# Performance work log

Measured on AMD Instinct MI355X. Metric: run time of the kernel, lower is better.

Reference implementation:

```python
import jax, jax.numpy as jnp
import numpy as np

_SAMPLING_EPS = 1e-05
_RMAX = 0.9999999403953552          # largest float32 uniform from tl.rand
_RMAX_LOG = -5.960464477539063e-08  # log(_RMAX)


def setup_inputs() -> dict:
    key = jax.random.key(0)
    k1, k2, k3, k4, k5 = jax.random.split(key, 5)
    B, V = 256, 128000
    logits = jax.random.normal(k1, (B, V), dtype=jnp.float32) * 4.0
    temperature = jax.random.uniform(k2, (B,), dtype=jnp.float32, minval=0.1, maxval=1.5)
    top_k = jax.random.randint(k3, (B,), 1, 1000).astype(jnp.int32)
    top_p = jax.random.uniform(k4, (B,), dtype=jnp.float32, minval=0.5, maxval=1.0)
    gumbel_u = jax.random.uniform(k5, (B, V), dtype=jnp.float32)
    return {
        "logits": logits,
        "temperature": temperature,
        "top_k": top_k,
        "top_p": top_p,
        "gumbel_u": gumbel_u,
        "num_logprobs": 20,
    }


def reference(logits, temperature, top_k, top_p, gumbel_u, num_logprobs):
    B, V = logits.shape
    # --- apply_temperature: divide by temp, temp<eps treated as 1.0 (greedy) ---
    temp = jnp.where(temperature < _SAMPLING_EPS, 1.0, temperature)
    logits = logits.astype(jnp.float32) / temp[:, None]

    # --- apply_top_k_top_p: sort ascending, mask, scatter back ---
    idx_sort = jnp.argsort(logits, axis=-1)                      # ascending
    logits_sort = jnp.take_along_axis(logits, idx_sort, axis=-1)
    # top-k: value of the k-th largest is at position V-k in ascending order
    k_pos = (V - top_k.astype(jnp.int32))[:, None]
    thresh = jnp.take_along_axis(logits_sort, k_pos, axis=-1)    # [B,1]
    logits_sort = jnp.where(logits_sort < thresh, -jnp.inf, logits_sort)
    # top-p: drop ascending prefix whose cumulative prob <= 1-p (keep last)
    probs_sort = jax.nn.softmax(logits_sort, axis=-1)
    cum = jnp.cumsum(probs_sort, axis=-1)
    mask_p = cum <= (1.0 - top_p)[:, None]
    mask_p = mask_p.at[:, -1].set(False)
    logits_sort = jnp.where(mask_p, -jnp.inf, logits_sort)
    # unsort back to vocab order
    inv = jnp.argsort(idx_sort, axis=-1)
    logits_f = jnp.take_along_axis(logits_sort, inv, axis=-1)

    # --- softmax + gumbel-trick sampling: argmax(p / -log(u)) ---
    probs = jax.nn.softmax(logits_f, axis=-1)
    q = -jnp.where(gumbel_u >= _RMAX, _RMAX_LOG, jnp.log(gumbel_u))
    greedy = (temperature < _SAMPLING_EPS)[:, None]  # kernel skips these rows
    ratio = jnp.where(greedy, probs, probs / q)
    sampled = jnp.argmax(ratio, axis=-1)             # [B]

    # --- gather_logprobs ---
    logprobs = jax.nn.log_softmax(logits_f, axis=-1)
    sampled_lp = jnp.take_along_axis(logprobs, sampled[:, None], axis=-1)  # [B,1]
    ranks = jnp.sum(logprobs > sampled_lp, axis=-1)                        # [B]
    topk_lp, topk_idx = jax.lax.top_k(logprobs, num_logprobs)
    indices = jnp.concatenate([sampled[:, None], topk_idx], axis=1)        # [B,1+K]
    lp_vals = jnp.concatenate([sampled_lp, topk_lp], axis=1)               # [B,1+K]

    return sampled[:, None], indices, lp_vals, ranks
```

## Files before the change

kernel.cpp:

```cpp
#include <hip/hip_runtime.h>
#include <math.h>

#define NTHR 1024
#define CAP 8192
#define BINS 4096
#define SMALL 1024
#define GUARD 16u
#define SS 4096

#define RMAX_F 0.9999999403953552f
#define RMAX_LOG_F -5.960464477539063e-08f
#define NEG_BIG -3.0e38f

__device__ __forceinline__ unsigned keyOf(float v) {
    unsigned b = __float_as_uint(v);
    return (b & 0x80000000u) ? ~b : (b | 0x80000000u);
}
__device__ __forceinline__ float valOfKey(unsigned k) {
    unsigned b = (k & 0x80000000u) ? (k ^ 0x80000000u) : ~k;
    return __uint_as_float(b);
}
__device__ __forceinline__ unsigned long long shflXor64(unsigned long long v, int m) {
    int lo = __shfl_xor((int)(unsigned)v, m);
    int hi = __shfl_xor((int)(unsigned)(v >> 32), m);
    return ((unsigned long long)(unsigned)hi << 32) | (unsigned)lo;
}

__global__ __launch_bounds__(NTHR) void sampler_kernel(
    const float* __restrict__ logits,
    const float* __restrict__ temperature,
    const int* __restrict__ top_kv,
    const float* __restrict__ top_pv,
    const float* __restrict__ gumbel,
    float* __restrict__ out,
    int B, int V, int K)
{
    const int r = blockIdx.x;
    const int tid = threadIdx.x;
    const int lane = tid & 63;
    const int wid = tid >> 6;

    __shared__ unsigned long long cand[CAP];
    __shared__ unsigned long long cand2[SMALL];
    __shared__ unsigned refHist[512];
    __shared__ int wtotI[16];
    __shared__ float varr[1024];
    __shared__ float Earr[1024];
    __shared__ float sfx[1024];
    __shared__ unsigned char flagArr[1024];
    __shared__ unsigned bitmap[64];
    __shared__ unsigned s_prefix;
    __shared__ int s_cntgt, s_total, s_lvl;
    __shared__ int s_ncand, s_nc2, s_nkeep, s_rank, s_g0, s_g1;
    __shared__ unsigned long long s_amax;
    __shared__ float s_vs;

    unsigned* hist = (unsigned*)cand;

    const float* row = logits + (long long)r * V;
    const float* urow = gumbel + (long long)r * V;

    float traw = temperature[r];
    bool greedy = traw < 1e-5f;
    float t = greedy ? 1.0f : traw;
    int k = top_kv[r];
    if (k < 1) k = 1;
    if (k > V) k = V;
    float p = top_pv[r];

    const float4* row4 = (const float4*)row;
    const int V4 = V >> 2;
    const int Vt = V4 << 2;
    const unsigned cpy = tid & 1u;

#define H4(v4) do { \
        atomicAdd(&hist[((keyOf((v4).x) >> 20) << 1) | cpy], 1u); \
        atomicAdd(&hist[((keyOf((v4).y) >> 20) << 1) | cpy], 1u); \
        atomicAdd(&hist[((keyOf((v4).z) >> 20) << 1) | cpy], 1u); \
        atomicAdd(&hist[((keyOf((v4).w) >> 20) << 1) | cpy], 1u); \
    } while (0)
#define SPEC1(val, gidx_, thr_) do { \
        float _v = (val); \
        if (_v >= (thr_)) { \
            int _pos = atomicAdd(&s_ncand, 1); \
            if (_pos < CAP) \
                cand[_pos] = ((unsigned long long)keyOf(_v) << 32) | (unsigned)(~(unsigned)(gidx_)); \
        } \
    } while (0)

    for (int i = tid; i < BINS * 2; i += NTHR) hist[i] = 0;
    __syncthreads();
    {
        int f4pos = (int)(((long long)tid * V4) >> 10);
        float4 sv = row4[f4pos];
        H4(sv);
    }
    __syncthreads();
    int ts;
    {
        int tc = 3 * k + 500;
        if (tc > 3500) tc = 3500;
        if (tc < 700) tc = 700;
        ts = (int)(((long long)tc * SS + V - 1) / V);
        if (ts < 4) ts = 4;
    }
    {
        int base = tid << 2;
        int cs = 0;
        #pragma unroll
        for (int j = 0; j < 4; ++j)
            cs += (int)(hist[(base + j) * 2] + hist[(base + j) * 2 + 1]);
        int vv = cs;
        #pragma unroll
        for (int d = 1; d < 64; d <<= 1) {
            int o = __shfl_down(vv, d);
            if (lane + d < 64) vv += o;
        }
        if (lane == 0) wtotI[wid] = vv;
        __syncthreads();
        int off = 0;
        for (int w = wid + 1; w < 16; ++w) off += wtotI[w];
        int mine = vv + off;
        int above = mine - cs;
        if (mine >= ts && above < ts) {
            int run = above;
            for (int b = base + 3; b >= base; --b) {
                int mb = (int)(hist[b * 2] + hist[b * 2 + 1]);
                if (run + mb >= ts) { s_prefix = (unsigned)b; break; }
                run += mb;
            }
        }
        if (tid == 0) s_ncand = 0;
        __syncthreads();
    }
    unsigned tlo = s_prefix << 20;
    float thrF = valOfKey(tlo);

    {
        int i = tid;
        for (; i + 3 * NTHR < V4; i += 4 * NTHR) {
            float4 a = row4[i];
            float4 b = row4[i + NTHR];
            float4 c = row4[i + 2 * NTHR];
            float4 d = row4[i + 3 * NTHR];
            SPEC1(a.x, i * 4 + 0, thrF); SPEC1(a.y, i * 4 + 1, thrF);
            SPEC1(a.z, i * 4 + 2, thrF); SPEC1(a.w, i * 4 + 3, thrF);
            SPEC1(b.x, (i + NTHR) * 4 + 0, thrF); SPEC1(b.y, (i + NTHR) * 4 + 1, thrF);
            SPEC1(b.z, (i + NTHR) * 4 + 2, thrF); SPEC1(b.w, (i + NTHR) * 4 + 3, thrF);
            SPEC1(c.x, (i + 2 * NTHR) * 4 + 0, thrF); SPEC1(c.y, (i + 2 * NTHR) * 4 + 1, thrF);
            SPEC1(c.z, (i + 2 * NTHR) * 4 + 2, thrF); SPEC1(c.w, (i + 2 * NTHR) * 4 + 3, thrF);
            SPEC1(d.x, (i + 3 * NTHR) * 4 + 0, thrF); SPEC1(d.y, (i + 3 * NTHR) * 4 + 1, thrF);
            SPEC1(d.z, (i + 3 * NTHR) * 4 + 2, thrF); SPEC1(d.w, (i + 3 * NTHR) * 4 + 3, thrF);
        }
        for (; i < V4; i += NTHR) {
            float4 a = row4[i];
            SPEC1(a.x, i * 4 + 0, thrF); SPEC1(a.y, i * 4 + 1, thrF);
            SPEC1(a.z, i * 4 + 2, thrF); SPEC1(a.w, i * 4 + 3, thrF);
        }
        for (int ii = Vt + tid; ii < V; ii += NTHR)
            SPEC1(row[ii], ii, thrF);
    }
    __syncthreads();
    int ncand = s_ncand;
    const bool fastok = (ncand >= k && ncand <= CAP);

    if (!fastok) {
        for (int i = tid; i < BINS * 2; i += NTHR) hist[i] = 0;
        __syncthreads();
        {
            int i = tid;
            for (; i + 3 * NTHR < V4; i += 4 * NTHR) {
                float4 a = row4[i];
                float4 b = row4[i + NTHR];
                float4 c = row4[i + 2 * NTHR];
                float4 d = row4[i + 3 * NTHR];
                H4(a); H4(b); H4(c); H4(d);
            }
            for (; i < V4; i += NTHR) { float4 a = row4[i]; H4(a); }
            for (int ii = Vt + tid; ii < V; ii += NTHR)
                atomicAdd(&hist[((keyOf(row[ii]) >> 20) << 1) | cpy], 1u);
        }
        __syncthreads();
        {
            int base = tid << 2;
            int cs = 0;
            #pragma unroll
            for (int j = 0; j < 4; ++j)
                cs += (int)(hist[(base + j) * 2] + hist[(base + j) * 2 + 1]);
            int vv = cs;
            #pragma unroll
            for (int d = 1; d < 64; d <<= 1) {
                int o = __shfl_down(vv, d);
                if (lane + d < 64) vv += o;
            }
            if (lane == 0) wtotI[wid] = vv;
            __syncthreads();
            int off = 0;
            for (int w = wid + 1; w < 16; ++w) off += wtotI[w];
            int mine = vv + off;
            int above = mine - cs;
            if (mine >= k && above < k) {
                int run = above;
                for (int b = base + 3; b >= base; --b) {
                    int mb = (int)(hist[b * 2] + hist[b * 2 + 1]);
                    if (run + mb >= k) {
                        s_prefix = (unsigned)b; s_cntgt = run; s_total = run + mb; s_lvl = 0;
                        break;
                    }
                    run += mb;
                }
            }
        }
        for (int level = 1; level <= 2; ++level) {
            __syncthreads();
            if (s_total <= CAP) break;
            for (int i = tid; i < 512; i += NTHR) hist[i] = 0;
            __syncthreads();
            unsigned pfx = s_prefix;
            const int msh = 32 - (12 + 8 * (level - 1));
            const int bsh = msh - 8;
            for (int i = tid; i < V4; i += NTHR) {
                float4 l4 = row4[i];
                float vv4[4] = { l4.x, l4.y, l4.z, l4.w };
                #pragma unroll
                for (int j = 0; j < 4; ++j) {
                    unsigned key = keyOf(vv4[j]);
                    if ((key >> msh) == pfx)
                        atomicAdd(&hist[(((key >> bsh) & 255u) << 1) | cpy], 1u);
                }
            }
            for (int i = Vt + tid; i < V; i += NTHR) {
                unsigned key = keyOf(row[i]);
                if ((key >> msh) == pfx)
                    atomicAdd(&hist[(((key >> bsh) & 255u) << 1) | cpy], 1u);
            }
            __syncthreads();
            if (tid == 0) {
                int run = s_cntgt;
                for (int b = 255; b >= 0; --b) {
                    int mb = (int)(hist[b * 2] + hist[b * 2 + 1]);
                    if (run + mb >= k) {
                        s_prefix = (pfx << 8) | (unsigned)b; s_cntgt = run; s_total = run + mb;
                        break;
                    }
                    run += mb;
                }
                s_lvl = level;
            }
        }
        __syncthreads();
        tlo = s_prefix << (20 - 8 * s_lvl);
        thrF = valOfKey(tlo);
        if (tid == 0) s_ncand = 0;
        __syncthreads();
        {
            int i = tid;
            for (; i + 3 * NTHR < V4; i += 4 * NTHR) {
                float4 a = row4[i];
                float4 b = row4[i + NTHR];
                float4 c = row4[i + 2 * NTHR];
                float4 d = row4[i + 3 * NTHR];
                SPEC1(a.x, i * 4 + 0, thrF); SPEC1(a.y, i * 4 + 1, thrF);
                SPEC1(a.z, i * 4 + 2, thrF); SPEC1(a.w, i * 4 + 3, thrF);
                SPEC1(b.x, (i + NTHR) * 4 + 0, thrF); SPEC1(b.y, (i + NTHR) * 4 + 1, thrF);
                SPEC1(b.z, (i + NTHR) * 4 + 2, thrF); SPEC1(b.w, (i + NTHR) * 4 + 3, thrF);
                SPEC1(c.x, (i + 2 * NTHR) * 4 + 0, thrF); SPEC1(c.y, (i + 2 * NTHR) * 4 + 1, thrF);
                SPEC1(c.z, (i + 2 * NTHR) * 4 + 2, thrF); SPEC1(c.w, (i + 2 * NTHR) * 4 + 3, thrF);
                SPEC1(d.x, (i + 3 * NTHR) * 4 + 0, thrF); SPEC1(d.y, (i + 3 * NTHR) * 4 + 1, thrF);
                SPEC1(d.z, (i + 3 * NTHR) * 4 + 2, thrF); SPEC1(d.w, (i + 3 * NTHR) * 4 + 3, thrF);
            }
            for (; i < V4; i += NTHR) {
                float4 a = row4[i];
                SPEC1(a.x, i * 4 + 0, thrF); SPEC1(a.y, i * 4 + 1, thrF);
                SPEC1(a.z, i * 4 + 2, thrF); SPEC1(a.w, i * 4 + 3, thrF);
            }
            for (int ii = Vt + tid; ii < V; ii += NTHR)
                SPEC1(row[ii], ii, thrF);
        }
        __syncthreads();
        ncand = s_ncand;
        if (ncand > CAP) ncand = CAP;
        if (k > ncand) k = ncand;
    }
    if (k > ncand) k = ncand;

    bool fromC2 = false;
    bool bigSort = false;
    if (ncand > SMALL) {
        unsigned pfx; int run; int bb;
        if (fastok) { pfx = 0u; run = 0; bb = 32; }
        else { pfx = s_prefix; run = s_cntgt; bb = 20 - 8 * s_lvl; }
        while (bb > 0) {
            int step = (bb >= 8) ? 8 : bb;
            bb -= step;
            int nbins = 1 << step;
            for (int i = tid; i < nbins * 2; i += NTHR) refHist[i] = 0;
            __syncthreads();
            {
                int sh = bb + step;
                for (int i = tid; i < ncand; i += NTHR) {
                    unsigned key = (unsigned)(cand[i] >> 32);
                    bool in = (sh >= 32) || ((key >> sh) == pfx);
                    if (in)
                        atomicAdd(&refHist[(((key >> bb) & (unsigned)(nbins - 1)) << 1) | cpy], 1u);
                }
            }
            __syncthreads();
            int cnt = 0;
            if (tid < 256) cnt = (tid < nbins) ? (int)(refHist[tid * 2] + refHist[tid * 2 + 1]) : 0;
            int vv = cnt;
            #pragma unroll
            for (int d = 1; d < 64; d <<= 1) {
                int o = __shfl_down(vv, d);
                if (lane + d < 64) vv += o;
            }
            if (tid < 256 && lane == 0) wtotI[wid] = vv;
            __syncthreads();
            if (tid < 256) {
                int off = 0;
                for (int w = wid + 1; w < 4; ++w) off += wtotI[w];
                int incl = vv + off;
                int abv = incl - cnt;
                int kk = k - run;
                if (incl >= kk && abv < kk) {
                    s_prefix = (pfx << step) | (unsigned)tid;
                    s_cntgt = run + abv;
                }
            }
            __syncthreads();
            pfx = s_prefix;
            run = s_cntgt;
        }
        unsigned tref = (pfx >= tlo + GUARD) ? (pfx - GUARD) : tlo;
        if (tid == 0) s_nc2 = 0;
        __syncthreads();
        for (int i = tid; i < ncand; i += NTHR) {
            unsigned long long cv = cand[i];
            bool pred = ((unsigned)(cv >> 32) >= tref);
            unsigned long long mask = __ballot(pred ? 1 : 0);
            if (mask) {
                int leader = __ffsll(mask) - 1;
                int cnt2 = __popcll(mask);
                int bpos = 0;
                if (lane == leader) bpos = atomicAdd(&s_nc2, cnt2);
                bpos = __shfl(bpos, leader);
                if (pred) {
                    int pos = bpos + __popcll(mask & ((1ULL << lane) - 1ULL));
                    if (pos < SMALL) cand2[pos] = cv;
                }
            }
        }
        __syncthreads();
        int nc2 = s_nc2;
        if (nc2 <= SMALL) { ncand = nc2; fromC2 = true; }
        else bigSort = true;
    }

    if (!bigSort) {
        const unsigned long long* src = fromC2 ? cand2 : cand;
        unsigned long long v = (tid < ncand) ? src[tid] : 0ULL;
        #pragma unroll
        for (int size = 2; size <= SMALL; size <<= 1) {
            #pragma unroll
            for (int stride = size >> 1; stride > 0; stride >>= 1) {
                unsigned long long o;
                if (stride < 64) {
                    o = shflXor64(v, stride);
                } else {
                    cand[tid] = v;
                    __syncthreads();
                    o = cand[tid ^ stride];
                    __syncthreads();
                }
                bool takeMax = (((tid & size) == 0) == ((tid & stride) == 0));
                unsigned long long mx = (v > o) ? v : o;
                unsigned long long mn = (v > o) ? o : v;
                v = takeMax ? mx : mn;
            }
        }
        cand[tid] = v;
        varr[tid] = (tid < ncand) ? (valOfKey((unsigned)(v >> 32)) / t) : NEG_BIG;
        __syncthreads();
    } else {
        int P = 2; while (P < ncand) P <<= 1;
        for (int i = ncand + tid; i < P; i += NTHR) cand[i] = 0ULL;
        __syncthreads();
        for (int size = 2; size <= P; size <<= 1) {
            for (int stride = size >> 1; stride > 0; stride >>= 1) {
                for (int i = tid; i < P; i += NTHR) {
                    int j = i ^ stride;
                    if (j > i) {
                        unsigned long long a = cand[i], b = cand[j];
                        bool up = ((i & size) == 0);
                        bool sw = up ? (a < b) : (a > b);
                        if (sw) { cand[i] = b; cand[j] = a; }
                    }
                }
                __syncthreads();
            }
        }
        for (int i = tid; i < 1024; i += NTHR)
            varr[i] = (i < ncand) ? (valOfKey((unsigned)(cand[i] >> 32)) / t) : NEG_BIG;
        __syncthreads();
    }

    const float m = varr[0];
    const float tkeyV = varr[k - 1];
    int ntop = k;
    while (ntop < ncand) {
        float vi = (ntop < 1024) ? varr[ntop]
                                 : (valOfKey((unsigned)(cand[ntop] >> 32)) / t);
        if (vi != tkeyV) break;
        ++ntop;
    }
    if (ntop > 1024) ntop = 1024;

    {
        float e = (tid < ntop) ? expf(varr[tid] - m) : 0.0f;
        Earr[tid] = e;
        sfx[tid] = e;
    }
    __syncthreads();
    for (int d = 1; d < 1024; d <<= 1) {
        float t0 = (tid + d < 1024) ? sfx[tid + d] : 0.0f;
        __syncthreads();
        sfx[tid] += t0;
        __syncthreads();
    }
    const float Zp = sfx[0];
    const float cmp = 1.0f - p;
    if (tid == 0) { s_nkeep = 0; s_rank = 0; s_amax = 0ULL; }
    for (int i = tid; i < 64; i += NTHR) bitmap[i] = 0;
    __syncthreads();
    {
        int local = 0;
        for (int i = tid; i < ntop; i += NTHR)
            if (sfx[i] / Zp > cmp) local++;
        #pragma unroll
        for (int d = 1; d < 64; d <<= 1) local += __shfl_xor(local, d);
        if (lane == 0 && local) atomicAdd(&s_nkeep, local);
    }
    __syncthreads();
    const int nkeep = s_nkeep;
    if (tid == 0) {
        float vb = varr[nkeep - 1];
        int g0 = nkeep - 1;
        while (g0 > 0 && varr[g0 - 1] == vb) --g0;
        int g1 = nkeep;
        while (g1 < ntop && varr[g1] == vb) ++g1;
        s_g0 = g0; s_g1 = g1;
    }
    __syncthreads();
    const int g0 = s_g0, g1 = s_g1;
    const int mkeep = nkeep - g0;
    for (int i = g0 + tid; i < g1; i += NTHR) {
        unsigned gi = ~(unsigned)(cand[i] & 0xFFFFFFFFull);
        int rk = 0;
        for (int j = g0; j < g1; ++j) {
            unsigned gj = ~(unsigned)(cand[j] & 0xFFFFFFFFull);
            if (gj > gi) rk++;
        }
        flagArr[i] = (rk < mkeep) ? 1 : 0;
    }
    __syncthreads();

    const float Z2 = (nkeep < 1024) ? (Zp - sfx[nkeep]) : Zp;
    const float L = logf(Z2);

    {
        unsigned long long lm = 0ULL;
        for (int i = tid; i < g1; i += NTHR) {
            if (i < g0 || flagArr[i]) {
                unsigned lo = (unsigned)(cand[i] & 0xFFFFFFFFull);
                unsigned gidx = ~lo;
                float u = urow[gidx];
                float q = -((u >= RMAX_F) ? RMAX_LOG_F : logf(u));
                float prob = Earr[i] / Z2;
                float ratio = greedy ? prob : (prob / q);
                unsigned long long comp = ((unsigned long long)__float_as_uint(ratio) << 32) | lo;
                if (comp > lm) lm = comp;
                if (gidx < 2048) atomicOr(&bitmap[gidx >> 5], 1u << (gidx & 31));
            }
        }
        #pragma unroll
        for (int d = 1; d < 64; d <<= 1) {
            unsigned long long o = shflXor64(lm, d);
            if (o > lm) lm = o;
        }
        if (lane == 0 && lm) atomicMax(&s_amax, lm);
    }
    __syncthreads();
    const unsigned samp_lo = (unsigned)(s_amax & 0xFFFFFFFFull);
    const unsigned samp = ~samp_lo;
    for (int i = tid; i < ntop; i += NTHR)
        if ((unsigned)(cand[i] & 0xFFFFFFFFull) == samp_lo) s_vs = varr[i];
    __syncthreads();
    const float lp_s = (s_vs - m) - L;
    {
        int local = 0;
        for (int i = tid; i < nkeep; i += NTHR)
            if ((varr[i] - m) - L > lp_s) local++;
        #pragma unroll
        for (int d = 1; d < 64; d <<= 1) local += __shfl_xor(local, d);
        if (lane == 0 && local) atomicAdd(&s_rank, local);
    }
    __syncthreads();

    float* o_samp = out;
    float* o_idx  = out + B;
    float* o_lp   = out + B + (long long)B * (K + 1);
    float* o_rank = out + B + 2LL * B * (K + 1);
    const long long rowo = (long long)r * (K + 1);
    const int ntk = (nkeep < K) ? nkeep : K;

    if (tid < g1) {
        const int i = tid;
        bool kept = (i < g0) || flagArr[i];
        if (kept) {
            float v = varr[i];
            int rs, re, base;
            if (i >= g0) { rs = g0; re = g1; base = g0; }
            else {
                rs = i; while (rs > 0 && varr[rs - 1] == v) --rs;
                re = i + 1; while (re < g1 && varr[re] == v) ++re;
                base = rs;
            }
            if (base < ntk) {
                unsigned myidx = ~(unsigned)(cand[i] & 0xFFFFFFFFull);
                int cnt = 0;
                for (int j = rs; j < re; ++j) {
                    if (j == i) continue;
                    if (j >= g0 && !flagArr[j]) continue;
                    unsigned gj = ~(unsigned)(cand[j] & 0xFFFFFFFFull);
                    if (gj < myidx) cnt++;
                }
                int slot = base + cnt;
                if (slot < ntk) {
                    o_idx[rowo + 1 + slot] = (float)myidx;
                    o_lp[rowo + 1 + slot] = (v - m) - L;
                }
            }
        }
    }

    if (tid == 0) {
        o_samp[r] = (float)samp;
        o_idx[rowo] = (float)samp;
        o_lp[rowo] = lp_s;
        o_rank[r] = (float)s_rank;
        if (nkeep < K) {
            int j = 0;
            for (int c = nkeep; c < K; ++c) {
                while (bitmap[j >> 5] & (1u << (j & 31))) ++j;
                o_idx[rowo + 1 + c] = (float)j;
                o_lp[rowo + 1 + c] = NEG_BIG;
                ++j;
            }
        }
    }
}

extern "C" void kernel_launch(void* const* d_in, const int* in_sizes, int n_in,
                              void* d_out, int out_size, void* d_ws, size_t ws_size,
                              hipStream_t stream) {
    const float* logits      = (const float*)d_in[0];
    const float* temperature = (const float*)d_in[1];
    const int*   top_k       = (const int*)d_in[2];
    const float* top_p       = (const float*)d_in[3];
    const float* gumbel      = (const float*)d_in[4];
    int B = in_sizes[1];
    int V = in_sizes[0] / B;
    int K = (out_size / B - 4) / 2;
    sampler_kernel<<<B, NTHR, 0, stream>>>(logits, temperature, top_k, top_p,
                                           gumbel, (float*)d_out, B, V, K);
}
```

Before: 268.0 us.

## Cut barriers and contention in candidate refinement, bitonic sort and suffix scan

Lowers the speculative candidate-count target so fewer elements pass the first threshold. The radix refinement histogram now uses 16 padded per-lane-group copies instead of 2, and the loop exits early once the surviving bucket fits the small sort. The block-wide bitonic stages double-buffer shared memory, and the suffix scan ping-pongs between two arrays, each dropping one barrier per step. Risks are more fallback passes when the smaller candidate target misses, extra shared memory that may lower occupancy, and a changed reference threshold when the refinement stops early.

```diff
diff --git a/kernel.cpp b/kernel.cpp
--- a/kernel.cpp
+++ b/kernel.cpp
@@ -42,11 +42,12 @@
 
     __shared__ unsigned long long cand[CAP];
     __shared__ unsigned long long cand2[SMALL];
-    __shared__ unsigned refHist[512];
+    __shared__ unsigned refHist[16 * 257];
     __shared__ int wtotI[16];
     __shared__ float varr[1024];
     __shared__ float Earr[1024];
     __shared__ float sfx[1024];
+    __shared__ float sfx2[1024];
     __shared__ unsigned char flagArr[1024];
     __shared__ unsigned bitmap[64];
     __shared__ unsigned s_prefix;
@@ -98,9 +99,9 @@
     __syncthreads();
     int ts;
     {
-        int tc = 3 * k + 500;
-        if (tc > 3500) tc = 3500;
-        if (tc < 700) tc = 700;
+        int tc = 2 * k + 400;
+        if (tc > 2400) tc = 2400;
+        if (tc < 600) tc = 600;
         ts = (int)(((long long)tc * SS + V - 1) / V);
         if (ts < 4) ts = 4;
     }
@@ -290,24 +291,29 @@
         unsigned pfx; int run; int bb;
         if (fastok) { pfx = 0u; run = 0; bb = 32; }
         else { pfx = s_prefix; run = s_cntgt; bb = 20 - 8 * s_lvl; }
-        while (bb > 0) {
+        int totR = ncand;
+        while (totR > SMALL - 16 && bb > 0) {
             int step = (bb >= 8) ? 8 : bb;
             bb -= step;
             int nbins = 1 << step;
-            for (int i = tid; i < nbins * 2; i += NTHR) refHist[i] = 0;
+            for (int i = tid; i < 16 * 257; i += NTHR) refHist[i] = 0;
             __syncthreads();
             {
-                int sh = bb + step;
+                const int sh = bb + step;
+                const unsigned lc = (unsigned)(lane & 15) * 257u;
                 for (int i = tid; i < ncand; i += NTHR) {
                     unsigned key = (unsigned)(cand[i] >> 32);
                     bool in = (sh >= 32) || ((key >> sh) == pfx);
                     if (in)
-                        atomicAdd(&refHist[(((key >> bb) & (unsigned)(nbins - 1)) << 1) | cpy], 1u);
+                        atomicAdd(&refHist[lc + ((key >> bb) & (unsigned)(nbins - 1))], 1u);
                 }
             }
             __syncthreads();
             int cnt = 0;
-            if (tid < 256) cnt = (tid < nbins) ? (int)(refHist[tid * 2] + refHist[tid * 2 + 1]) : 0;
+            if (tid < 256 && tid < nbins) {
+                #pragma unroll
+                for (int c = 0; c < 16; ++c) cnt += (int)refHist[c * 257 + tid];
+            }
             int vv = cnt;
             #pragma unroll
             for (int d = 1; d < 64; d <<= 1) {
@@ -325,13 +331,16 @@
                 if (incl >= kk && abv < kk) {
                     s_prefix = (pfx << step) | (unsigned)tid;
                     s_cntgt = run + abv;
+                    s_total = run + abv + cnt;
                 }
             }
             __syncthreads();
             pfx = s_prefix;
             run = s_cntgt;
-        }
-        unsigned tref = (pfx >= tlo + GUARD) ? (pfx - GUARD) : tlo;
+            totR = s_total;
+        }
+        unsigned tref0 = (bb > 0) ? (pfx << bb) : pfx;
+        unsigned tref = (tref0 >= GUARD) ? (tref0 - GUARD) : 0u;
         if (tid == 0) s_nc2 = 0;
         __syncthreads();
         for (int i = tid; i < ncand; i += NTHR) {
@@ -359,6 +368,7 @@
     if (!bigSort) {
         const unsigned long long* src = fromC2 ? cand2 : cand;
         unsigned long long v = (tid < ncand) ? src[tid] : 0ULL;
+        int seg = 0;
         #pragma unroll
         for (int size = 2; size <= SMALL; size <<= 1) {
             #pragma unroll
@@ -367,10 +377,10 @@
                 if (stride < 64) {
                     o = shflXor64(v, stride);
                 } else {
-                    cand[tid] = v;
+                    cand[seg * SMALL + tid] = v;
                     __syncthreads();
-                    o = cand[tid ^ stride];
-                    __syncthreads();
+                    o = cand[seg * SMALL + (tid ^ stride)];
+                    seg ^= 1;
                 }
                 bool takeMax = (((tid & size) == 0) == ((tid & stride) == 0));
                 unsigned long long mx = (v > o) ? v : o;
@@ -419,19 +429,23 @@
         float e = (tid < ntop) ? expf(varr[tid] - m) : 0.0f;
         Earr[tid] = e;
         sfx[tid] = e;
-    }
-    __syncthreads();
-    for (int d = 1; d < 1024; d <<= 1) {
-        float t0 = (tid + d < 1024) ? sfx[tid + d] : 0.0f;
-        __syncthreads();
-        sfx[tid] += t0;
-        __syncthreads();
+        if (tid == 0) { s_nkeep = 0; s_rank = 0; s_amax = 0ULL; }
+        if (tid < 64) bitmap[tid] = 0;
+    }
+    __syncthreads();
+    {
+        float* A = sfx;
+        float* Bf = sfx2;
+        #pragma unroll
+        for (int d = 1; d < 1024; d <<= 1) {
+            float t0 = (tid + d < 1024) ? A[tid + d] : 0.0f;
+            Bf[tid] = A[tid] + t0;
+            __syncthreads();
+            float* tmp = A; A = Bf; Bf = tmp;
+        }
     }
     const float Zp = sfx[0];
     const float cmp = 1.0f - p;
-    if (tid == 0) { s_nkeep = 0; s_rank = 0; s_amax = 0ULL; }
-    for (int i = tid; i < 64; i += NTHR) bitmap[i] = 0;
-    __syncthreads();
     {
         int local = 0;
         for (int i = tid; i < ntop; i += NTHR)
```

After: 265.4 us. Within noise of the previous version (-1.0%).
